# Performance work log

Hardware: AMD Instinct MI355X
Metric: run time of the kernel (lower is better)

## Reference

```python
import jax, jax.numpy as jnp
import numpy as np

N = 50000
E = 800000
IN_CH = 128
OUT_CH = 128
HEADS = 4
HEAD_DIM = OUT_CH // HEADS  # 32
NEG_SLOPE = 0.2
BN_EPS = 1e-5


def setup_inputs() -> dict:
    key = jax.random.key(0)
    ks = jax.random.split(key, 12)
    s = 1.0 / np.sqrt(IN_CH)
    x = jax.random.normal(ks[0], (N, IN_CH), dtype=jnp.float32)
    edge_index = jax.random.randint(ks[1], (2, E), 0, N, dtype=jnp.int64)
    # GATv2 lin_l (source) and lin_r (target) weights + biases
    W_l = jax.random.uniform(ks[2], (IN_CH, HEADS * HEAD_DIM), jnp.float32, -s, s)
    b_l = jax.random.uniform(ks[3], (HEADS * HEAD_DIM,), jnp.float32, -s, s)
    W_r = jax.random.uniform(ks[4], (IN_CH, HEADS * HEAD_DIM), jnp.float32, -s, s)
    b_r = jax.random.uniform(ks[5], (HEADS * HEAD_DIM,), jnp.float32, -s, s)
    att = jax.random.uniform(ks[6], (HEADS, HEAD_DIM), jnp.float32, -s, s)
    bias = jnp.zeros((HEADS * HEAD_DIM,), jnp.float32)
    gamma = jnp.ones((OUT_CH,), jnp.float32)
    beta = jnp.zeros((OUT_CH,), jnp.float32)
    return {"x": x, "edge_index": edge_index, "W_l": W_l, "b_l": b_l,
            "W_r": W_r, "b_r": b_r, "att": att, "bias": bias,
            "gamma": gamma, "beta": beta}


def gatv2_layer(x, edge_index, W_l, b_l, W_r, b_r, att, bias, gamma, beta):
    # transformed source/target features: [N, H, C]
    x_l = (x @ W_l + b_l).reshape(N, HEADS, HEAD_DIM)
    x_r = (x @ W_r + b_r).reshape(N, HEADS, HEAD_DIM)
    # add self loops
    loop = jnp.arange(N, dtype=edge_index.dtype)
    src = jnp.concatenate([edge_index[0], loop])
    dst = jnp.concatenate([edge_index[1], loop])
    # GATv2 attention scores per edge: a^T LeakyReLU(x_j + x_i)  -> [Etot, H]
    e = jax.nn.leaky_relu(x_l[src] + x_r[dst], NEG_SLOPE)
    score = jnp.einsum('ehc,hc->eh', e, att)
    # segment softmax over incoming edges of each destination node
    m = jax.ops.segment_max(score, dst, num_segments=N)
    ex = jnp.exp(score - m[dst])
    denom = jax.ops.segment_sum(ex, dst, num_segments=N)
    alpha = ex / denom[dst]
    # scatter-add aggregation of alpha * x_l[src]
    out = jax.ops.segment_sum(alpha[:, :, None] * x_l[src], dst, num_segments=N)
    out = out.reshape(N, OUT_CH) + bias
    # BatchNorm over nodes (training-mode batch statistics)
    mu = jnp.mean(out, axis=0)
    var = jnp.var(out, axis=0)
    out = (out - mu) / jnp.sqrt(var + BN_EPS) * gamma + beta
    # residual (in_channels == out_channels -> identity path) + ELU
    out = jax.nn.elu(out + x)
    return out


def reference(x, edge_index, W_l, b_l, W_r, b_r, att, bias, gamma, beta):
    return gatv2_layer(x, edge_index, W_l, b_l, W_r, b_r, att, bias, gamma, beta)
```

## Files before the change

### kernel.cpp

```cpp
#include <hip/hip_runtime.h>

#define NN 50000
#define EE 800000
#define ETOT (EE + NN)
#define GEMM_GRID 391
#define MTILES 782
#define COUNT_BLOCKS 3125
#define AGG_BLOCKS 1280
#define SCAN_BLOCKS 196

typedef __attribute__((ext_vector_type(8))) short bhalf8;
typedef __attribute__((ext_vector_type(4))) float fx4;

__device__ __forceinline__ unsigned bf16r(float f) {
  unsigned u = __float_as_uint(f);
  return (u + 0x7FFFu + ((u >> 16) & 1u)) >> 16;
}

__device__ __forceinline__ float4 unpack_bf16x4(unsigned a, unsigned b) {
  float4 f;
  f.x = __uint_as_float(a << 16);
  f.y = __uint_as_float(a & 0xFFFF0000u);
  f.z = __uint_as_float(b << 16);
  f.w = __uint_as_float(b & 0xFFFF0000u);
  return f;
}

#define GLOAD_LDS16(gp, lp)                                          \
  __builtin_amdgcn_global_load_lds(                                  \
      (const __attribute__((address_space(1))) void*)(gp),           \
      (__attribute__((address_space(3))) void*)(lp), 16, 0, 0)

__global__ __launch_bounds__(256) void gemm_count(
    const float* __restrict__ x,
    const float* __restrict__ Wl, const float* __restrict__ bl,
    const float* __restrict__ Wr, const float* __restrict__ br,
    unsigned short* __restrict__ xlh, float* __restrict__ xr,
    const int* __restrict__ ei, int* __restrict__ deg) {
  if (blockIdx.x >= GEMM_GRID) {
    int e = (blockIdx.x - GEMM_GRID) * 256 + threadIdx.x;
    if (e < EE) atomicAdd(&deg[ei[EE + e]], 1);
    return;
  }
  __shared__ unsigned short sW[256 * 136];
  const int t = threadIdx.x;
  const int w = t >> 6;
  const int l = t & 63;
  const int cl = l & 15;
  const int kb = (l >> 4) * 8;
  const int rsub = (l >> 4) * 4;

#pragma unroll
  for (int it = 0; it < 16; ++it) {
    int f4 = t + it * 256;
    int k = f4 >> 5;
    int c4 = (f4 & 31) * 4;
    float4 v = *(const float4*)&Wl[(size_t)k * 128 + c4];
    sW[(c4 + 0) * 136 + k] = (unsigned short)bf16r(v.x);
    sW[(c4 + 1) * 136 + k] = (unsigned short)bf16r(v.y);
    sW[(c4 + 2) * 136 + k] = (unsigned short)bf16r(v.z);
    sW[(c4 + 3) * 136 + k] = (unsigned short)bf16r(v.w);
    float4 u = *(const float4*)&Wr[(size_t)k * 128 + c4];
    sW[(128 + c4 + 0) * 136 + k] = (unsigned short)bf16r(u.x);
    sW[(128 + c4 + 1) * 136 + k] = (unsigned short)bf16r(u.y);
    sW[(128 + c4 + 2) * 136 + k] = (unsigned short)bf16r(u.z);
    sW[(128 + c4 + 3) * 136 + k] = (unsigned short)bf16r(u.w);
  }
  __syncthreads();

  bhalf8 bfr[4][4];
  float biasv[4];
#pragma unroll
  for (int nt = 0; nt < 4; ++nt) {
    int col = w * 64 + nt * 16 + cl;
    biasv[nt] = (col < 128) ? bl[col] : br[col - 128];
#pragma unroll
    for (int ch = 0; ch < 4; ++ch)
      bfr[nt][ch] = *(const bhalf8*)&sW[col * 136 + ch * 32 + kb];
  }

  for (int mt = blockIdx.x; mt < MTILES; mt += GEMM_GRID) {
    const int m0 = mt * 64;
#pragma unroll
    for (int rt = 0; rt < 4; ++rt) {
      int row = m0 + rt * 16 + cl;
      int rowc = row < NN ? row : NN - 1;
      const float* xp = x + (size_t)rowc * 128 + kb;
      bhalf8 afr[4];
#pragma unroll
      for (int ch = 0; ch < 4; ++ch) {
        float4 q0 = *(const float4*)(xp + ch * 32);
        float4 q1 = *(const float4*)(xp + ch * 32 + 4);
        bhalf8 f;
        f[0] = (short)bf16r(q0.x); f[1] = (short)bf16r(q0.y);
        f[2] = (short)bf16r(q0.z); f[3] = (short)bf16r(q0.w);
        f[4] = (short)bf16r(q1.x); f[5] = (short)bf16r(q1.y);
        f[6] = (short)bf16r(q1.z); f[7] = (short)bf16r(q1.w);
        afr[ch] = f;
      }
#pragma unroll
      for (int nt = 0; nt < 4; ++nt) {
        fx4 acc = {biasv[nt], biasv[nt], biasv[nt], biasv[nt]};
#pragma unroll
        for (int ch = 0; ch < 4; ++ch)
          acc = __builtin_amdgcn_mfma_f32_16x16x32_bf16(afr[ch], bfr[nt][ch],
                                                        acc, 0, 0, 0);
        int col = w * 64 + nt * 16 + cl;
        int rbase = m0 + rt * 16 + rsub;
        if (col < 128) {
#pragma unroll
          for (int r = 0; r < 4; ++r) {
            int rr = rbase + r;
            if (rr < NN) xlh[(size_t)rr * 128 + col] = (unsigned short)bf16r(acc[r]);
          }
        } else {
          int c2 = col - 128;
#pragma unroll
          for (int r = 0; r < 4; ++r) {
            int rr = rbase + r;
            if (rr < NN) xr[(size_t)rr * 128 + c2] = acc[r];
          }
        }
      }
    }
  }
}

__global__ __launch_bounds__(256) void scanA(const int* __restrict__ deg,
                                             int* __restrict__ bsum,
                                             float* __restrict__ bn) {
  __shared__ int s[256];
  int t = threadIdx.x;
  if (blockIdx.x == 0) bn[t] = 0.f;
  int i = blockIdx.x * 256 + t;
  s[t] = (i < NN) ? deg[i] : 0;
  __syncthreads();
#pragma unroll
  for (int off = 128; off > 0; off >>= 1) {
    if (t < off) s[t] += s[t + off];
    __syncthreads();
  }
  if (t == 0) bsum[blockIdx.x] = s[0];
}

__global__ __launch_bounds__(256) void scanB(const int* __restrict__ deg,
                                             const int* __restrict__ bsum,
                                             int* __restrict__ offs,
                                             int* __restrict__ cursor) {
  __shared__ int s[256];
  __shared__ int bpref;
  int t = threadIdx.x;
  int bid = blockIdx.x;
  int i = bid * 256 + t;
  int v = (i < NN) ? deg[i] : 0;
  s[t] = v;
  if (t == 0) {
    int r = 0;
    for (int k = 0; k < bid; ++k) r += bsum[k];
    bpref = r;
  }
  __syncthreads();
  for (int off = 1; off < 256; off <<= 1) {
    int u = (t >= off) ? s[t - off] : 0;
    __syncthreads();
    s[t] += u;
    __syncthreads();
  }
  int excl = s[t] - v + bpref;
  if (i <= NN) {
    offs[i] = excl;
    if (i < NN) cursor[i] = excl;
  }
}

__global__ void fill_csr(const int* __restrict__ ei, int* __restrict__ cursor,
                         int* __restrict__ csr) {
  int e = blockIdx.x * 256 + threadIdx.x;
  if (e >= ETOT) return;
  int s, d;
  if (e < EE) { s = ei[e]; d = ei[EE + e]; }
  else { s = e - EE; d = s; }
  int pos = atomicAdd(&cursor[d], 1);
  csr[pos] = s;
}

__global__ __launch_bounds__(256, 8) void aggregate(
    const unsigned short* __restrict__ xlh, const float* __restrict__ xr,
    const int* __restrict__ offs, const int* __restrict__ csr,
    const float* __restrict__ att, float* __restrict__ out) {
  __shared__ __align__(16) unsigned char stg[4][8][1024];
  const int t = threadIdx.x;
  const int w = t >> 6;
  const int l = t & 63;
  const int g = l >> 4;
  const int gl = l & 15;
  const int gb = l & 48;
  const int c8 = gl * 8;
  unsigned char* wbase = &stg[w][0][0];
  const float4 at0 = *(const float4*)&att[c8];
  const float4 at1 = *(const float4*)&att[c8 + 4];
  const int wgid = blockIdx.x * 4 + w;
  const int nstride = gridDim.x * 16;

  for (int nb = wgid * 4; nb < NN; nb += nstride) {
    const int node = nb + g;
    const int nodec = node < NN ? node : NN - 1;
    const float4 xr0 = *(const float4*)&xr[(size_t)nodec * 128 + c8];
    const float4 xr1 = *(const float4*)&xr[(size_t)nodec * 128 + c8 + 4];
    const int beg = offs[nodec];
    int deg = offs[nodec + 1] - beg;
    if (node >= NN) deg = 0;
    int maxd = deg;
    maxd = max(maxd, __shfl_xor(maxd, 16));
    maxd = max(maxd, __shfl_xor(maxd, 32));

    int m0, m1, m2, m3;
    { int a = beg + gl;      a = a < ETOT ? a : ETOT - 1; m0 = csr[a]; }
    m1 = m0; m2 = m0; m3 = m0;
    if (maxd > 16) { int a = beg + 16 + gl; a = a < ETOT ? a : ETOT - 1; m1 = csr[a]; }
    if (maxd > 32) { int a = beg + 32 + gl; a = a < ETOT ? a : ETOT - 1; m2 = csr[a]; }
    if (maxd > 48) { int a = beg + 48 + gl; a = a < ETOT ? a : ETOT - 1; m3 = csr[a]; }

    float xtouch = xr0.x + xr1.x;
    asm volatile("" :: "v"(xtouch));

    float den = 0.f;
    float4 a0 = make_float4(0, 0, 0, 0), a1 = make_float4(0, 0, 0, 0);

#define STAGE(i) do {                                                      \
      int ii = (i);                                                        \
      int cr = ii < 16 ? m0 : ii < 32 ? m1 : ii < 48 ? m2 : m3;            \
      int s = __shfl(cr, gb + (ii & 15), 64);                              \
      if (ii >= deg) s = 0;                                                \
      GLOAD_LDS16(xlh + (size_t)s * 128 + c8,                              \
                  wbase + (((unsigned)(ii)&7u) << 10));                    \
    } while (0)

#define CONSUME(i) do {                                                    \
      uint4 u = *(const uint4*)(wbase + (((unsigned)(i)&7u) << 10) + l * 16); \
      float4 v0 = unpack_bf16x4(u.x, u.y);                                 \
      float4 v1 = unpack_bf16x4(u.z, u.w);                                 \
      float e, p;                                                          \
      e = v0.x + xr0.x; e = e > 0.f ? e : 0.2f * e; p = e * at0.x;         \
      e = v0.y + xr0.y; e = e > 0.f ? e : 0.2f * e; p = fmaf(e, at0.y, p); \
      e = v0.z + xr0.z; e = e > 0.f ? e : 0.2f * e; p = fmaf(e, at0.z, p); \
      e = v0.w + xr0.w; e = e > 0.f ? e : 0.2f * e; p = fmaf(e, at0.w, p); \
      e = v1.x + xr1.x; e = e > 0.f ? e : 0.2f * e; p = fmaf(e, at1.x, p); \
      e = v1.y + xr1.y; e = e > 0.f ? e : 0.2f * e; p = fmaf(e, at1.y, p); \
      e = v1.z + xr1.z; e = e > 0.f ? e : 0.2f * e; p = fmaf(e, at1.z, p); \
      e = v1.w + xr1.w; e = e > 0.f ? e : 0.2f * e; p = fmaf(e, at1.w, p); \
      p += __shfl_xor(p, 1);                                               \
      p += __shfl_xor(p, 2);                                               \
      float pe = ((i) < deg) ? __expf(p) : 0.f;                            \
      den += pe;                                                           \
      a0.x = fmaf(pe, v0.x, a0.x); a0.y = fmaf(pe, v0.y, a0.y);            \
      a0.z = fmaf(pe, v0.z, a0.z); a0.w = fmaf(pe, v0.w, a0.w);            \
      a1.x = fmaf(pe, v1.x, a1.x); a1.y = fmaf(pe, v1.y, a1.y);            \
      a1.z = fmaf(pe, v1.z, a1.z); a1.w = fmaf(pe, v1.w, a1.w);            \
    } while (0)

    const int mp = maxd < 64 ? maxd : 64;
    const int pro = mp < 7 ? mp : 7;
    for (int i = 0; i < pro; ++i) STAGE(i);
    const int me = mp - 7;
    for (int i = 0; i < me; ++i) {
      STAGE(i + 7);
      asm volatile("s_waitcnt vmcnt(7)" ::: "memory");
      CONSUME(i);
    }
    asm volatile("s_waitcnt vmcnt(0)" ::: "memory");
    for (int i = me > 0 ? me : 0; i < mp; ++i) CONSUME(i);

    for (int i = 64; i < maxd; ++i) {
      int a = beg + i; a = a < ETOT ? a : ETOT - 1;
      int s = csr[a];
      if (i >= deg) s = 0;
      uint4 u = *(const uint4*)(xlh + (size_t)s * 128 + c8);
      float4 v0 = unpack_bf16x4(u.x, u.y);
      float4 v1 = unpack_bf16x4(u.z, u.w);
      float e, p;
      e = v0.x + xr0.x; e = e > 0.f ? e : 0.2f * e; p = e * at0.x;
      e = v0.y + xr0.y; e = e > 0.f ? e : 0.2f * e; p = fmaf(e, at0.y, p);
      e = v0.z + xr0.z; e = e > 0.f ? e : 0.2f * e; p = fmaf(e, at0.z, p);
      e = v0.w + xr0.w; e = e > 0.f ? e : 0.2f * e; p = fmaf(e, at0.w, p);
      e = v1.x + xr1.x; e = e > 0.f ? e : 0.2f * e; p = fmaf(e, at1.x, p);
      e = v1.y + xr1.y; e = e > 0.f ? e : 0.2f * e; p = fmaf(e, at1.y, p);
      e = v1.z + xr1.z; e = e > 0.f ? e : 0.2f * e; p = fmaf(e, at1.z, p);
      e = v1.w + xr1.w; e = e > 0.f ? e : 0.2f * e; p = fmaf(e, at1.w, p);
      p += __shfl_xor(p, 1);
      p += __shfl_xor(p, 2);
      float pe = (i < deg) ? __expf(p) : 0.f;
      den += pe;
      a0.x = fmaf(pe, v0.x, a0.x); a0.y = fmaf(pe, v0.y, a0.y);
      a0.z = fmaf(pe, v0.z, a0.z); a0.w = fmaf(pe, v0.w, a0.w);
      a1.x = fmaf(pe, v1.x, a1.x); a1.y = fmaf(pe, v1.y, a1.y);
      a1.z = fmaf(pe, v1.z, a1.z); a1.w = fmaf(pe, v1.w, a1.w);
    }
#undef STAGE
#undef CONSUME

    if (node < NN) {
      float inv = 1.0f / den;
      float4 r0, r1;
      r0.x = a0.x * inv; r0.y = a0.y * inv; r0.z = a0.z * inv; r0.w = a0.w * inv;
      r1.x = a1.x * inv; r1.y = a1.y * inv; r1.z = a1.z * inv; r1.w = a1.w * inv;
      *(float4*)&out[(size_t)node * 128 + c8] = r0;
      *(float4*)&out[(size_t)node * 128 + c8 + 4] = r1;
    }
  }
}

__global__ __launch_bounds__(256) void bn_stats(const float* __restrict__ out,
                                                float* __restrict__ bn) {
  __shared__ float sb[256];
  int t = threadIdx.x;
  sb[t] = 0.f;
  __syncthreads();
  const int c4 = (t & 31) * 4;
  float4 s = make_float4(0, 0, 0, 0), q = make_float4(0, 0, 0, 0);
  const int total4 = NN * 32;
  for (int i = blockIdx.x * 256 + t; i < total4; i += gridDim.x * 256) {
    float4 o = ((const float4*)out)[i];
    s.x += o.x; s.y += o.y; s.z += o.z; s.w += o.w;
    q.x += o.x * o.x; q.y += o.y * o.y; q.z += o.z * o.z; q.w += o.w * o.w;
  }
  atomicAdd(&sb[c4 + 0], s.x);
  atomicAdd(&sb[c4 + 1], s.y);
  atomicAdd(&sb[c4 + 2], s.z);
  atomicAdd(&sb[c4 + 3], s.w);
  atomicAdd(&sb[128 + c4 + 0], q.x);
  atomicAdd(&sb[128 + c4 + 1], q.y);
  atomicAdd(&sb[128 + c4 + 2], q.z);
  atomicAdd(&sb[128 + c4 + 3], q.w);
  __syncthreads();
  atomicAdd(&bn[t], sb[t]);
}

__global__ __launch_bounds__(256) void finalize(
    float* __restrict__ out, const float* __restrict__ x,
    const float* __restrict__ bn, const float* __restrict__ gamma,
    const float* __restrict__ beta) {
  __shared__ float smu[128], sgi[128];
  int t = threadIdx.x;
  if (t < 128) {
    float mu = bn[t] * (1.0f / NN);
    float var = bn[128 + t] * (1.0f / NN) - mu * mu;
    smu[t] = mu;
    sgi[t] = rsqrtf(var + 1e-5f) * gamma[t];
  }
  __syncthreads();
  const int total4 = NN * 32;
  for (int i = blockIdx.x * blockDim.x + threadIdx.x; i < total4;
       i += gridDim.x * blockDim.x) {
    int c4 = (i & 31) * 4;
    float4 o = ((const float4*)out)[i];
    float4 xv = ((const float4*)x)[i];
    float4 mu = *(const float4*)&smu[c4];
    float4 gi = *(const float4*)&sgi[c4];
    float4 b4 = *(const float4*)&beta[c4];
    float v;
    v = (o.x - mu.x) * gi.x + b4.x + xv.x; o.x = v > 0.f ? v : expm1f(v);
    v = (o.y - mu.y) * gi.y + b4.y + xv.y; o.y = v > 0.f ? v : expm1f(v);
    v = (o.z - mu.z) * gi.z + b4.z + xv.z; o.z = v > 0.f ? v : expm1f(v);
    v = (o.w - mu.w) * gi.w + b4.w + xv.w; o.w = v > 0.f ? v : expm1f(v);
    ((float4*)out)[i] = o;
  }
}

extern "C" void kernel_launch(void* const* d_in, const int* in_sizes, int n_in,
                              void* d_out, int out_size, void* d_ws, size_t ws_size,
                              hipStream_t stream) {
  const float* x    = (const float*)d_in[0];
  const int*   ei   = (const int*)d_in[1];
  const float* Wl   = (const float*)d_in[2];
  const float* bl   = (const float*)d_in[3];
  const float* Wr   = (const float*)d_in[4];
  const float* br   = (const float*)d_in[5];
  const float* att  = (const float*)d_in[6];
  const float* gam  = (const float*)d_in[8];
  const float* bet  = (const float*)d_in[9];
  float* out = (float*)d_out;

  unsigned short* xlh = (unsigned short*)d_ws;
  float* xr   = (float*)(xlh + (size_t)NN * 128);
  int* offs   = (int*)(xr + (size_t)NN * 128);
  int* cursor = offs + (NN + 4);
  int* deg    = cursor + NN;
  int* csr    = deg + NN;
  float* bn   = (float*)(csr + ETOT);
  int* bsum   = (int*)(bn + 256);

  hipMemsetD32Async((hipDeviceptr_t)deg, 1, NN, stream);

  hipLaunchKernelGGL(gemm_count, dim3(GEMM_GRID + COUNT_BLOCKS), dim3(256), 0,
                     stream, x, Wl, bl, Wr, br, xlh, xr, ei, deg);
  hipLaunchKernelGGL(scanA, dim3(SCAN_BLOCKS), dim3(256), 0, stream, deg, bsum, bn);
  hipLaunchKernelGGL(scanB, dim3(SCAN_BLOCKS), dim3(256), 0, stream,
                     deg, bsum, offs, cursor);
  hipLaunchKernelGGL(fill_csr, dim3((ETOT + 255) / 256), dim3(256), 0, stream,
                     ei, cursor, csr);
  hipLaunchKernelGGL(aggregate, dim3(AGG_BLOCKS), dim3(256), 0, stream,
                     xlh, xr, offs, csr, att, out);
  hipLaunchKernelGGL(bn_stats, dim3(1024), dim3(256), 0, stream, out, bn);
  hipLaunchKernelGGL(finalize, dim3(2048), dim3(256), 0, stream, out, x, bn, gam, bet);
}
```

Measured before the change: 313.0 us.

## Prefetch next node's metadata in aggregate loop, use DPP quad reduction

```diff
diff --git a/kernel.cpp b/kernel.cpp
--- a/kernel.cpp
+++ b/kernel.cpp
@@ -24,6 +24,12 @@
   f.z = __uint_as_float(b << 16);
   f.w = __uint_as_float(b & 0xFFFF0000u);
   return f;
+}
+
+__device__ __forceinline__ float quad_red(float p) {
+  p += __int_as_float(__builtin_amdgcn_mov_dpp(__float_as_int(p), 0xB1, 0xF, 0xF, true));
+  p += __int_as_float(__builtin_amdgcn_mov_dpp(__float_as_int(p), 0x4E, 0xF, 0xF, true));
+  return p;
 }
 
 #define GLOAD_LDS16(gp, lp)                                          \
@@ -202,25 +208,24 @@
   const int wgid = blockIdx.x * 4 + w;
   const int nstride = gridDim.x * 16;
 
-  for (int nb = wgid * 4; nb < NN; nb += nstride) {
-    const int node = nb + g;
-    const int nodec = node < NN ? node : NN - 1;
-    const float4 xr0 = *(const float4*)&xr[(size_t)nodec * 128 + c8];
-    const float4 xr1 = *(const float4*)&xr[(size_t)nodec * 128 + c8 + 4];
-    const int beg = offs[nodec];
-    int deg = offs[nodec + 1] - beg;
-    if (node >= NN) deg = 0;
-    int maxd = deg;
-    maxd = max(maxd, __shfl_xor(maxd, 16));
-    maxd = max(maxd, __shfl_xor(maxd, 32));
-
-    int m0, m1, m2, m3;
-    { int a = beg + gl;      a = a < ETOT ? a : ETOT - 1; m0 = csr[a]; }
-    m1 = m0; m2 = m0; m3 = m0;
-    if (maxd > 16) { int a = beg + 16 + gl; a = a < ETOT ? a : ETOT - 1; m1 = csr[a]; }
-    if (maxd > 32) { int a = beg + 32 + gl; a = a < ETOT ? a : ETOT - 1; m2 = csr[a]; }
-    if (maxd > 48) { int a = beg + 48 + gl; a = a < ETOT ? a : ETOT - 1; m3 = csr[a]; }
-
+  int nb = wgid * 4;
+  int node = nb + g;
+  int nodec = node < NN ? node : NN - 1;
+  float4 xr0 = *(const float4*)&xr[(size_t)nodec * 128 + c8];
+  float4 xr1 = *(const float4*)&xr[(size_t)nodec * 128 + c8 + 4];
+  int beg = offs[nodec];
+  int deg = offs[nodec + 1] - beg;
+  if (node >= NN) deg = 0;
+  int maxd = deg;
+  maxd = max(maxd, __shfl_xor(maxd, 16));
+  maxd = max(maxd, __shfl_xor(maxd, 32));
+  int m0, m1, m2, m3;
+  { int a = beg + gl;      a = a < ETOT ? a : ETOT - 1; m0 = csr[a]; }
+  { int a = beg + 16 + gl; a = a < ETOT ? a : ETOT - 1; m1 = csr[a]; }
+  { int a = beg + 32 + gl; a = a < ETOT ? a : ETOT - 1; m2 = csr[a]; }
+  { int a = beg + 48 + gl; a = a < ETOT ? a : ETOT - 1; m3 = csr[a]; }
+
+  for (; nb < NN; nb += nstride) {
     float xtouch = xr0.x + xr1.x;
     asm volatile("" :: "v"(xtouch));
 
@@ -241,16 +246,15 @@
       float4 v0 = unpack_bf16x4(u.x, u.y);                                 \
       float4 v1 = unpack_bf16x4(u.z, u.w);                                 \
       float e, p;                                                          \
-      e = v0.x + xr0.x; e = e > 0.f ? e : 0.2f * e; p = e * at0.x;         \
-      e = v0.y + xr0.y; e = e > 0.f ? e : 0.2f * e; p = fmaf(e, at0.y, p); \
-      e = v0.z + xr0.z; e = e > 0.f ? e : 0.2f * e; p = fmaf(e, at0.z, p); \
-      e = v0.w + xr0.w; e = e > 0.f ? e : 0.2f * e; p = fmaf(e, at0.w, p); \
-      e = v1.x + xr1.x; e = e > 0.f ? e : 0.2f * e; p = fmaf(e, at1.x, p); \
-      e = v1.y + xr1.y; e = e > 0.f ? e : 0.2f * e; p = fmaf(e, at1.y, p); \
-      e = v1.z + xr1.z; e = e > 0.f ? e : 0.2f * e; p = fmaf(e, at1.z, p); \
-      e = v1.w + xr1.w; e = e > 0.f ? e : 0.2f * e; p = fmaf(e, at1.w, p); \
-      p += __shfl_xor(p, 1);                                               \
-      p += __shfl_xor(p, 2);                                               \
+      e = v0.x + xr0.x; e = fmaxf(e, 0.2f * e); p = e * at0.x;             \
+      e = v0.y + xr0.y; e = fmaxf(e, 0.2f * e); p = fmaf(e, at0.y, p);     \
+      e = v0.z + xr0.z; e = fmaxf(e, 0.2f * e); p = fmaf(e, at0.z, p);     \
+      e = v0.w + xr0.w; e = fmaxf(e, 0.2f * e); p = fmaf(e, at0.w, p);     \
+      e = v1.x + xr1.x; e = fmaxf(e, 0.2f * e); p = fmaf(e, at1.x, p);     \
+      e = v1.y + xr1.y; e = fmaxf(e, 0.2f * e); p = fmaf(e, at1.y, p);     \
+      e = v1.z + xr1.z; e = fmaxf(e, 0.2f * e); p = fmaf(e, at1.z, p);     \
+      e = v1.w + xr1.w; e = fmaxf(e, 0.2f * e); p = fmaf(e, at1.w, p);     \
+      p = quad_red(p);                                                     \
       float pe = ((i) < deg) ? __expf(p) : 0.f;                            \
       den += pe;                                                           \
       a0.x = fmaf(pe, v0.x, a0.x); a0.y = fmaf(pe, v0.y, a0.y);            \
@@ -268,6 +272,21 @@
       asm volatile("s_waitcnt vmcnt(7)" ::: "memory");
       CONSUME(i);
     }
+
+    const int nb2 = nb + nstride;
+    int node2 = nb2 + g;
+    int nodec2 = node2 < NN ? node2 : NN - 1;
+    float4 nxr0 = *(const float4*)&xr[(size_t)nodec2 * 128 + c8];
+    float4 nxr1 = *(const float4*)&xr[(size_t)nodec2 * 128 + c8 + 4];
+    int beg2 = offs[nodec2];
+    int deg2 = offs[nodec2 + 1] - beg2;
+    if (node2 >= NN) deg2 = 0;
+    int n0, n1, n2, n3;
+    { int a = beg2 + gl;      a = a < ETOT ? a : ETOT - 1; n0 = csr[a]; }
+    { int a = beg2 + 16 + gl; a = a < ETOT ? a : ETOT - 1; n1 = csr[a]; }
+    { int a = beg2 + 32 + gl; a = a < ETOT ? a : ETOT - 1; n2 = csr[a]; }
+    { int a = beg2 + 48 + gl; a = a < ETOT ? a : ETOT - 1; n3 = csr[a]; }
+
     asm volatile("s_waitcnt vmcnt(0)" ::: "memory");
     for (int i = me > 0 ? me : 0; i < mp; ++i) CONSUME(i);
 
@@ -279,16 +298,15 @@
       float4 v0 = unpack_bf16x4(u.x, u.y);
       float4 v1 = unpack_bf16x4(u.z, u.w);
       float e, p;
-      e = v0.x + xr0.x; e = e > 0.f ? e : 0.2f * e; p = e * at0.x;
-      e = v0.y + xr0.y; e = e > 0.f ? e : 0.2f * e; p = fmaf(e, at0.y, p);
-      e = v0.z + xr0.z; e = e > 0.f ? e : 0.2f * e; p = fmaf(e, at0.z, p);
-      e = v0.w + xr0.w; e = e > 0.f ? e : 0.2f * e; p = fmaf(e, at0.w, p);
-      e = v1.x + xr1.x; e = e > 0.f ? e : 0.2f * e; p = fmaf(e, at1.x, p);
-      e = v1.y + xr1.y; e = e > 0.f ? e : 0.2f * e; p = fmaf(e, at1.y, p);
-      e = v1.z + xr1.z; e = e > 0.f ? e : 0.2f * e; p = fmaf(e, at1.z, p);
-      e = v1.w + xr1.w; e = e > 0.f ? e : 0.2f * e; p = fmaf(e, at1.w, p);
-      p += __shfl_xor(p, 1);
-      p += __shfl_xor(p, 2);
+      e = v0.x + xr0.x; e = fmaxf(e, 0.2f * e); p = e * at0.x;
+      e = v0.y + xr0.y; e = fmaxf(e, 0.2f * e); p = fmaf(e, at0.y, p);
+      e = v0.z + xr0.z; e = fmaxf(e, 0.2f * e); p = fmaf(e, at0.z, p);
+      e = v0.w + xr0.w; e = fmaxf(e, 0.2f * e); p = fmaf(e, at0.w, p);
+      e = v1.x + xr1.x; e = fmaxf(e, 0.2f * e); p = fmaf(e, at1.x, p);
+      e = v1.y + xr1.y; e = fmaxf(e, 0.2f * e); p = fmaf(e, at1.y, p);
+      e = v1.z + xr1.z; e = fmaxf(e, 0.2f * e); p = fmaf(e, at1.z, p);
+      e = v1.w + xr1.w; e = fmaxf(e, 0.2f * e); p = fmaf(e, at1.w, p);
+      p = quad_red(p);
       float pe = (i < deg) ? __expf(p) : 0.f;
       den += pe;
       a0.x = fmaf(pe, v0.x, a0.x); a0.y = fmaf(pe, v0.y, a0.y);
@@ -307,6 +325,14 @@
       *(float4*)&out[(size_t)node * 128 + c8] = r0;
       *(float4*)&out[(size_t)node * 128 + c8 + 4] = r1;
     }
+
+    int maxd2 = deg2;
+    maxd2 = max(maxd2, __shfl_xor(maxd2, 16));
+    maxd2 = max(maxd2, __shfl_xor(maxd2, 32));
+
+    xr0 = nxr0; xr1 = nxr1;
+    m0 = n0; m1 = n1; m2 = n2; m3 = n3;
+    beg = beg2; deg = deg2; maxd = maxd2; node = node2;
   }
 }
 
```

After: 306.3 us. 2.1% less time.
